# Kernel tuning notes

Hardware: AMD Instinct MI355X
Metric: run time of the kernel (lower is better)

## Reference

```python
import jax, jax.numpy as jnp
import numpy as np

N_NODES = 100000
N_EDGES = 1600000
D_FEAT = 64


def setup_inputs() -> dict:
    key = jax.random.key(0)
    k1, k2, k3, k4 = jax.random.split(key, 4)
    inp = jax.random.normal(k1, (N_NODES, D_FEAT), dtype=jnp.float32)
    adj_vals = jax.random.uniform(k2, (N_EDGES,), dtype=jnp.float32)
    adj_rows = jax.random.randint(k3, (N_EDGES,), 0, N_NODES, dtype=jnp.int32)
    adj_cols = jax.random.randint(k4, (N_EDGES,), 0, N_NODES, dtype=jnp.int32)
    return {"input": inp, "adj_vals": adj_vals, "adj_rows": adj_rows, "adj_cols": adj_cols}


def reference(input, adj_vals, adj_rows, adj_cols):
    # SpMM: out = A @ H with A in COO form. out[i] = sum_e vals[e] * H[cols[e]] for rows[e]==i
    msgs = adj_vals[:, None] * jnp.take(input, adj_cols, axis=0)  # [E, D]
    out = jax.ops.segment_sum(msgs, adj_rows, num_segments=N_NODES)  # [N, D]
    return out
```

## Files before the change

kernel.cpp:

```cpp
#include <hip/hip_runtime.h>

#define N_NODES 100000
#define N_EDGES 1600000
#define D_FEAT 64

#define N_PART 8
#define SLICE  (N_EDGES / N_PART)

#define RB_LOG 7
#define ROWS_PER_BUCKET 128
#define N_BUCKET ((N_NODES + ROWS_PER_BUCKET - 1) / ROWS_PER_BUCKET)
#define N_CELL (N_BUCKET * N_PART)

#define COL_BITS 17
#define COL_MASK ((1 << COL_BITS) - 1)

#define MAXREC 3072

__global__ __launch_bounds__(256) void hist_kernel(
    const int* __restrict__ rows, int* __restrict__ histG)
{
    __shared__ int h[N_BUCKET];
    for (int i = threadIdx.x; i < N_BUCKET; i += 256) h[i] = 0;
    __syncthreads();

    int part = blockIdx.x & (N_PART - 1);
    int blk  = blockIdx.x >> 3;
    int nblk = gridDim.x >> 3;
    int base = part * SLICE;

    for (int e = blk * 256 + threadIdx.x; e < SLICE; e += nblk * 256)
        atomicAdd(&h[rows[base + e] >> RB_LOG], 1);
    __syncthreads();

    for (int i = threadIdx.x; i < N_BUCKET; i += 256)
        if (h[i]) atomicAdd(&histG[part * N_BUCKET + i], h[i]);
}

__global__ __launch_bounds__(1024) void scan_kernel(
    const int* __restrict__ histG, int* __restrict__ cellptr,
    int* __restrict__ cursor)
{
    const int PER = 8;
    __shared__ int buf[2][1024];
    int t = threadIdx.x;

    int pre[PER];
    int s = 0;
    #pragma unroll
    for (int j = 0; j < PER; ++j) {
        int cm = t * PER + j;
        int x = 0;
        if (cm < N_CELL) x = histG[(cm & (N_PART - 1)) * N_BUCKET + (cm >> 3)];
        pre[j] = s; s += x;
    }
    buf[0][t] = s;
    __syncthreads();
    int src = 0;
    for (int off = 1; off < 1024; off <<= 1) {
        int dst = 1 - src;
        int x = buf[src][t];
        if (t >= off) x += buf[src][t - off];
        buf[dst][t] = x;
        __syncthreads();
        src = dst;
    }
    int offset = buf[src][t] - s;
    #pragma unroll
    for (int j = 0; j < PER; ++j) {
        int cm = t * PER + j;
        if (cm < N_CELL) {
            int val = offset + pre[j];
            cellptr[cm] = val;
            cursor[(cm & (N_PART - 1)) * N_BUCKET + (cm >> 3)] = val;
        }
    }
    if (t == 0) cellptr[N_CELL] = N_EDGES;
}

__global__ __launch_bounds__(256) void scatter_kernel(
    const float* __restrict__ vals, const int* __restrict__ rows,
    const int* __restrict__ cols, int* __restrict__ cursor,
    int2* __restrict__ rec)
{
    int part = blockIdx.x & (N_PART - 1);
    int blk  = blockIdx.x >> 3;
    int nblk = gridDim.x >> 3;
    int base = part * SLICE;
    int* cur = cursor + part * N_BUCKET;

    for (int e = blk * 256 + threadIdx.x; e < SLICE; e += nblk * 256) {
        int idx = base + e;
        int r = rows[idx];
        int b = r >> RB_LOG;
        int pos = atomicAdd(&cur[b], 1);
        int packed = ((r & (ROWS_PER_BUCKET - 1)) << COL_BITS) | cols[idx];
        rec[pos] = make_int2(packed, __float_as_int(vals[idx]));
    }
}

__global__ __launch_bounds__(256) void gather_kernel(
    const float* __restrict__ H, const int2* __restrict__ rec,
    const int* __restrict__ cellptr, float* __restrict__ out)
{
    __shared__ int2           recbuf[MAXREC];
    __shared__ unsigned short order[MAXREC];
    __shared__ int            rstart[ROWS_PER_BUCKET + 1];
    __shared__ int            rcur[ROWS_PER_BUCKET];
    __shared__ int            sbuf[2][ROWS_PER_BUCKET];

    int b = blockIdx.x;
    int start = cellptr[b * N_PART];
    int end   = cellptr[b * N_PART + N_PART];

    int tid = threadIdx.x;
    int rg = tid >> 4;
    int fc = tid & 15;
    const float4* H4 = reinterpret_cast<const float4*>(H);

    float4 acc[8];
    #pragma unroll
    for (int k = 0; k < 8; ++k) acc[k] = make_float4(0.f, 0.f, 0.f, 0.f);

    for (int base = start; base < end; base += MAXREC) {
        int n = min(end - base, MAXREC);

        if (tid < ROWS_PER_BUCKET) rcur[tid] = 0;
        __syncthreads();

        for (int i = tid; i < n; i += 256) {
            int2 r = rec[base + i];
            recbuf[i] = r;
            atomicAdd(&rcur[r.x >> COL_BITS], 1);
        }
        __syncthreads();

        if (tid < ROWS_PER_BUCKET) sbuf[0][tid] = rcur[tid];
        __syncthreads();
        int src = 0;
        for (int off = 1; off < ROWS_PER_BUCKET; off <<= 1) {
            if (tid < ROWS_PER_BUCKET) {
                int x = sbuf[src][tid];
                if (tid >= off) x += sbuf[src][tid - off];
                sbuf[1 - src][tid] = x;
            }
            __syncthreads();
            src ^= 1;
        }
        if (tid < ROWS_PER_BUCKET) rstart[tid + 1] = sbuf[src][tid];
        if (tid == 0) rstart[0] = 0;
        __syncthreads();
        if (tid < ROWS_PER_BUCKET) rcur[tid] = rstart[tid];
        __syncthreads();

        for (int i = tid; i < n; i += 256) {
            int ro = recbuf[i].x >> COL_BITS;
            int pos = atomicAdd(&rcur[ro], 1);
            order[pos] = (unsigned short)i;
        }
        __syncthreads();

        #pragma unroll
        for (int k = 0; k < 8; ++k) {
            int ro = k * 16 + rg;
            int s = rstart[ro], e2 = rstart[ro + 1];
            int i = s;
            for (; i + 2 <= e2; i += 2) {
                int j0 = order[i], j1 = order[i + 1];
                int2 r0 = recbuf[j0];
                int2 r1 = recbuf[j1];
                float4 h0 = H4[(r0.x & COL_MASK) * 16 + fc];
                float4 h1 = H4[(r1.x & COL_MASK) * 16 + fc];
                float v0 = __int_as_float(r0.y);
                float v1 = __int_as_float(r1.y);
                acc[k].x += v0 * h0.x; acc[k].y += v0 * h0.y;
                acc[k].z += v0 * h0.z; acc[k].w += v0 * h0.w;
                acc[k].x += v1 * h1.x; acc[k].y += v1 * h1.y;
                acc[k].z += v1 * h1.z; acc[k].w += v1 * h1.w;
            }
            if (i < e2) {
                int j0 = order[i];
                int2 r0 = recbuf[j0];
                float4 h0 = H4[(r0.x & COL_MASK) * 16 + fc];
                float v0 = __int_as_float(r0.y);
                acc[k].x += v0 * h0.x; acc[k].y += v0 * h0.y;
                acc[k].z += v0 * h0.z; acc[k].w += v0 * h0.w;
            }
        }
        __syncthreads();
    }

    int rowbase = b * ROWS_PER_BUCKET;
    #pragma unroll
    for (int k = 0; k < 8; ++k) {
        int row = rowbase + k * 16 + rg;
        if (row < N_NODES)
            reinterpret_cast<float4*>(out)[row * 16 + fc] = acc[k];
    }
}

extern "C" void kernel_launch(void* const* d_in, const int* in_sizes, int n_in,
                              void* d_out, int out_size, void* d_ws, size_t ws_size,
                              hipStream_t stream) {
    const float* H    = (const float*)d_in[0];
    const float* vals = (const float*)d_in[1];
    const int*   rows = (const int*)d_in[2];
    const int*   cols = (const int*)d_in[3];
    float* out = (float*)d_out;

    char* ws = (char*)d_ws;
    int2* rec     = (int2*)ws;
    int*  histG   = (int*)(rec + N_EDGES);
    int*  cursor  = histG + N_PART * N_BUCKET;
    int*  cellptr = cursor + N_PART * N_BUCKET;

    hipMemsetAsync(histG, 0, N_PART * N_BUCKET * sizeof(int), stream);

    hist_kernel<<<512, 256, 0, stream>>>(rows, histG);
    scan_kernel<<<1, 1024, 0, stream>>>(histG, cellptr, cursor);
    scatter_kernel<<<512, 256, 0, stream>>>(vals, rows, cols, cursor, rec);
    gather_kernel<<<N_BUCKET, 256, 0, stream>>>(H, rec, cellptr, out);
}
```

Before: 252.4 us.

## Pad per-bucket cursors to separate cache lines, raise grid sizes, unroll gather by four

```diff
diff --git a/kernel.cpp b/kernel.cpp
--- a/kernel.cpp
+++ b/kernel.cpp
@@ -17,6 +17,8 @@
 
 #define MAXREC 3072
 
+#define PAD 16
+
 __global__ __launch_bounds__(256) void hist_kernel(
     const int* __restrict__ rows, int* __restrict__ histG)
 {
@@ -34,7 +36,7 @@
     __syncthreads();
 
     for (int i = threadIdx.x; i < N_BUCKET; i += 256)
-        if (h[i]) atomicAdd(&histG[part * N_BUCKET + i], h[i]);
+        if (h[i]) atomicAdd(&histG[(part * N_BUCKET + i) * PAD], h[i]);
 }
 
 __global__ __launch_bounds__(1024) void scan_kernel(
@@ -51,7 +53,8 @@
     for (int j = 0; j < PER; ++j) {
         int cm = t * PER + j;
         int x = 0;
-        if (cm < N_CELL) x = histG[(cm & (N_PART - 1)) * N_BUCKET + (cm >> 3)];
+        if (cm < N_CELL)
+            x = histG[((cm & (N_PART - 1)) * N_BUCKET + (cm >> 3)) * PAD];
         pre[j] = s; s += x;
     }
     buf[0][t] = s;
@@ -72,7 +75,7 @@
         if (cm < N_CELL) {
             int val = offset + pre[j];
             cellptr[cm] = val;
-            cursor[(cm & (N_PART - 1)) * N_BUCKET + (cm >> 3)] = val;
+            cursor[((cm & (N_PART - 1)) * N_BUCKET + (cm >> 3)) * PAD] = val;
         }
     }
     if (t == 0) cellptr[N_CELL] = N_EDGES;
@@ -87,13 +90,13 @@
     int blk  = blockIdx.x >> 3;
     int nblk = gridDim.x >> 3;
     int base = part * SLICE;
-    int* cur = cursor + part * N_BUCKET;
+    int* cur = cursor + part * N_BUCKET * PAD;
 
     for (int e = blk * 256 + threadIdx.x; e < SLICE; e += nblk * 256) {
         int idx = base + e;
         int r = rows[idx];
         int b = r >> RB_LOG;
-        int pos = atomicAdd(&cur[b], 1);
+        int pos = atomicAdd(&cur[b * PAD], 1);
         int packed = ((r & (ROWS_PER_BUCKET - 1)) << COL_BITS) | cols[idx];
         rec[pos] = make_int2(packed, __float_as_int(vals[idx]));
     }
@@ -165,20 +168,31 @@
             int ro = k * 16 + rg;
             int s = rstart[ro], e2 = rstart[ro + 1];
             int i = s;
-            for (; i + 2 <= e2; i += 2) {
+            for (; i + 4 <= e2; i += 4) {
                 int j0 = order[i], j1 = order[i + 1];
+                int j2 = order[i + 2], j3 = order[i + 3];
                 int2 r0 = recbuf[j0];
                 int2 r1 = recbuf[j1];
+                int2 r2 = recbuf[j2];
+                int2 r3 = recbuf[j3];
                 float4 h0 = H4[(r0.x & COL_MASK) * 16 + fc];
                 float4 h1 = H4[(r1.x & COL_MASK) * 16 + fc];
+                float4 h2 = H4[(r2.x & COL_MASK) * 16 + fc];
+                float4 h3 = H4[(r3.x & COL_MASK) * 16 + fc];
                 float v0 = __int_as_float(r0.y);
                 float v1 = __int_as_float(r1.y);
+                float v2 = __int_as_float(r2.y);
+                float v3 = __int_as_float(r3.y);
                 acc[k].x += v0 * h0.x; acc[k].y += v0 * h0.y;
                 acc[k].z += v0 * h0.z; acc[k].w += v0 * h0.w;
                 acc[k].x += v1 * h1.x; acc[k].y += v1 * h1.y;
                 acc[k].z += v1 * h1.z; acc[k].w += v1 * h1.w;
+                acc[k].x += v2 * h2.x; acc[k].y += v2 * h2.y;
+                acc[k].z += v2 * h2.z; acc[k].w += v2 * h2.w;
+                acc[k].x += v3 * h3.x; acc[k].y += v3 * h3.y;
+                acc[k].z += v3 * h3.z; acc[k].w += v3 * h3.w;
             }
-            if (i < e2) {
+            for (; i < e2; ++i) {
                 int j0 = order[i];
                 int2 r0 = recbuf[j0];
                 float4 h0 = H4[(r0.x & COL_MASK) * 16 + fc];
@@ -211,13 +225,13 @@
     char* ws = (char*)d_ws;
     int2* rec     = (int2*)ws;
     int*  histG   = (int*)(rec + N_EDGES);
-    int*  cursor  = histG + N_PART * N_BUCKET;
-    int*  cellptr = cursor + N_PART * N_BUCKET;
-
-    hipMemsetAsync(histG, 0, N_PART * N_BUCKET * sizeof(int), stream);
-
-    hist_kernel<<<512, 256, 0, stream>>>(rows, histG);
+    int*  cursor  = histG + N_CELL * PAD;
+    int*  cellptr = cursor + N_CELL * PAD;
+
+    hipMemsetAsync(histG, 0, N_CELL * PAD * sizeof(int), stream);
+
+    hist_kernel<<<1024, 256, 0, stream>>>(rows, histG);
     scan_kernel<<<1, 1024, 0, stream>>>(histG, cellptr, cursor);
-    scatter_kernel<<<512, 256, 0, stream>>>(vals, rows, cols, cursor, rec);
+    scatter_kernel<<<2048, 256, 0, stream>>>(vals, rows, cols, cursor, rec);
     gather_kernel<<<N_BUCKET, 256, 0, stream>>>(H, rec, cellptr, out);
 }
```

Measured after the change: 253.4 us. No clear change (+0.4%).
